# Kernel optimization log

Hardware: AMD Instinct MI355X
Metric: run time of the kernel (lower is better)

## Reference

```python
import jax, jax.numpy as jnp
import numpy as np

N_HEADS = 16
N_KV_HEADS = 4
HEAD_DIM = 128
D_MODEL = 2048
WINDOW = 1024
THETA = 10000.0
EPS = 1e-6


def _rmsnorm(x, w):
    var = jnp.mean(x * x, axis=-1, keepdims=True)
    return x * jax.lax.rsqrt(var + EPS) * w


def _rope(x, pos):
    # x: [B, H, S, D]; rotate-half (llama-style) RoPE
    d2 = HEAD_DIM // 2
    inv_freq = 1.0 / (THETA ** (jnp.arange(0, HEAD_DIM, 2, dtype=jnp.float32) / HEAD_DIM))
    ang = pos[:, None].astype(jnp.float32) * inv_freq[None, :]  # [S, D/2]
    cos = jnp.cos(ang)[None, None]
    sin = jnp.sin(ang)[None, None]
    x1, x2 = x[..., :d2], x[..., d2:]
    return jnp.concatenate([x1 * cos - x2 * sin, x1 * sin + x2 * cos], axis=-1)


def setup_inputs() -> dict:
    key = jax.random.key(0)
    ks = jax.random.split(key, 7)
    B, S = 1, 2048
    s = 0.02
    return {
        "x": jax.random.normal(ks[0], (B, S, D_MODEL), jnp.float32),
        "wq": jax.random.normal(ks[1], (N_HEADS * HEAD_DIM, D_MODEL), jnp.float32) * s,
        "wk": jax.random.normal(ks[2], (N_KV_HEADS * HEAD_DIM, D_MODEL), jnp.float32) * s,
        "wv": jax.random.normal(ks[3], (N_KV_HEADS * HEAD_DIM, D_MODEL), jnp.float32) * s,
        "wo": jax.random.normal(ks[4], (D_MODEL, N_HEADS * HEAD_DIM), jnp.float32) * s,
        "q_norm_w": jnp.ones((HEAD_DIM,), jnp.float32),
        "k_norm_w": jnp.ones((HEAD_DIM,), jnp.float32),
    }


def reference(x, wq, wk, wv, wo, q_norm_w, k_norm_w):
    B, S, _ = x.shape
    past_length = 0
    scale = HEAD_DIM ** -0.5
    n_rep = N_HEADS // N_KV_HEADS

    q = (x @ wq.T).reshape(B, S, N_HEADS, HEAD_DIM).transpose(0, 2, 1, 3)
    k = (x @ wk.T).reshape(B, S, N_KV_HEADS, HEAD_DIM).transpose(0, 2, 1, 3)
    v = (x @ wv.T).reshape(B, S, N_KV_HEADS, HEAD_DIM).transpose(0, 2, 1, 3)

    q = _rmsnorm(q, q_norm_w)
    k = _rmsnorm(k, k_norm_w)

    pos = jnp.arange(S) + past_length
    q = _rope(q, pos)
    k = _rope(k, pos)

    # GQA: materialize repeated KV heads, as in _repeat_kv
    k_rep = jnp.repeat(k, n_rep, axis=1)  # [B, H, S, D]
    v_rep = jnp.repeat(v, n_rep, axis=1)

    # sliding-window causal mask (total_seq_len=S > WINDOW)
    q_idx = jnp.arange(S)[:, None] + past_length
    k_idx = jnp.arange(S)[None, :]
    mask = (q_idx >= k_idx) & (q_idx - k_idx < WINDOW)  # [S, S]

    scores = jnp.einsum("bhqd,bhkd->bhqk", q, k_rep) * scale
    scores = jnp.where(mask[None, None], scores, jnp.float32(-jnp.inf))
    attn = jax.nn.softmax(scores, axis=-1)
    out = jnp.einsum("bhqk,bhkd->bhqd", attn, v_rep)

    out = out.transpose(0, 2, 1, 3).reshape(B, S, N_HEADS * HEAD_DIM)
    return out @ wo.T
```

## Files before the change

kernel.cpp:

```cpp
#include <hip/hip_runtime.h>
#include <hip/hip_bf16.h>
#include <cstdint>
#include <cstddef>

typedef __attribute__((ext_vector_type(4))) float f32x4;
typedef __attribute__((ext_vector_type(8))) short bf16x8;
typedef __attribute__((ext_vector_type(8))) unsigned short us8;

#define MFMA16(a, b, c) __builtin_amdgcn_mfma_f32_16x16x32_bf16(a, b, c, 0, 0, 0)

__device__ inline unsigned short f2bf(float f) {
    unsigned int u = __float_as_uint(f);
    u += 0x7fffu + ((u >> 16) & 1u);
    return (unsigned short)(u >> 16);
}
__device__ inline float bf2f(unsigned short u) {
    return __uint_as_float((unsigned int)u << 16);
}
__device__ inline unsigned short f2bf_fast(float f) {
    float r;
    asm("v_cvt_pk_bf16_f32 %0, %1, %2" : "=v"(r) : "v"(f), "v"(f));
    return (unsigned short)__float_as_uint(r);
}

__device__ inline void gload_lds16(const void* g, void* l) {
    __builtin_amdgcn_global_load_lds(
        (const __attribute__((address_space(1))) void*)g,
        (__attribute__((address_space(3))) void*)l, 16, 0, 0);
}
__device__ inline unsigned lds_addr(const void* p) {
    return (unsigned)(size_t)((__attribute__((address_space(3))) const void*)p);
}

__global__ __launch_bounds__(256) void prep_all(const float* __restrict__ x,
                                                const float* __restrict__ wq,
                                                const float* __restrict__ wk,
                                                const float* __restrict__ wv,
                                                const float* __restrict__ wo,
                                                unsigned short* __restrict__ xb,
                                                unsigned short* __restrict__ wqkv,
                                                unsigned short* __restrict__ wob,
                                                float2* __restrict__ tbl) {
    const int b = blockIdx.x;
    if (b < 14336) {
        const float* src; unsigned short* dst; int off4;
        if (b < 4096)       { src = x;  dst = xb;                 off4 = b; }
        else if (b < 8192)  { src = wq; dst = wqkv;               off4 = b - 4096; }
        else if (b < 9216)  { src = wk; dst = wqkv + 2048 * 2048; off4 = b - 8192; }
        else if (b < 10240) { src = wv; dst = wqkv + 2560 * 2048; off4 = b - 9216; }
        else                { src = wo; dst = wob;                off4 = b - 10240; }
        int i = (off4 * 256 + threadIdx.x) * 4;
        float4 v = *(const float4*)(src + i);
        ushort4 o;
        o.x = f2bf(v.x); o.y = f2bf(v.y); o.z = f2bf(v.z); o.w = f2bf(v.w);
        *(ushort4*)(dst + i) = o;
    } else {
        int idx = (b - 14336) * 256 + threadIdx.x;
        int row = idx >> 6, t = idx & 63;
        float inv_freq = exp2f((float)t * (-2.0f / 128.0f) * 13.287712379549449f);
        float s, c;
        sincosf((float)row * inv_freq, &s, &c);
        tbl[idx] = make_float2(c, s);
    }
}

__global__ __launch_bounds__(512, 1) void gemm256(const unsigned short* __restrict__ A,
                                                  const unsigned short* __restrict__ B,
                                                  unsigned short* __restrict__ Cp,
                                                  int M, int N, int Kfull, int kspan) {
    __shared__ unsigned short As[2][256 * 64];
    __shared__ unsigned short Bs[2][256 * 64];
    const int tid = threadIdx.x;
    const int lane = tid & 63, wave = tid >> 6;
    const int wr = wave >> 2, wc = wave & 3;
    const int l15 = lane & 15, l4 = lane >> 4;
    const int gx = gridDim.x;
    const int nwg = gx * gridDim.y;
    const int bid0 = blockIdx.y * gx + blockIdx.x;
    const int q8 = nwg >> 3, r8 = nwg & 7;
    const int xcd = bid0 & 7, sub = bid0 >> 3;
    const int wgid = ((xcd < r8) ? xcd * (q8 + 1) : r8 * (q8 + 1) + (xcd - r8) * q8) + sub;
    const int bm = wgid / gx, bn = wgid % gx;
    const int z = blockIdx.z;
    const unsigned short* Az = A + (size_t)z * kspan;
    const unsigned short* Bz = B + (size_t)z * kspan;
    unsigned short* C = Cp + (size_t)z * M * N;
    const int nK = kspan >> 6;

    f32x4 acc[8][4] = {};

    const int sA0 = tid, sA1 = 512 + tid, sA2 = 1024 + tid, sA3 = 1536 + tid;
#define SRCOF(s) ((((((s) & 7) * 16) ^ ((((s) >> 3) & 7) << 4)) >> 1))
    const unsigned short* pa0 = Az + (size_t)(bm * 256 + (sA0 >> 3)) * Kfull + SRCOF(sA0);
    const unsigned short* pa1 = Az + (size_t)(bm * 256 + (sA1 >> 3)) * Kfull + SRCOF(sA1);
    const unsigned short* pa2 = Az + (size_t)(bm * 256 + (sA2 >> 3)) * Kfull + SRCOF(sA2);
    const unsigned short* pa3 = Az + (size_t)(bm * 256 + (sA3 >> 3)) * Kfull + SRCOF(sA3);
    const unsigned short* pb0 = Bz + (size_t)(bn * 256 + (sA0 >> 3)) * Kfull + SRCOF(sA0);
    const unsigned short* pb1 = Bz + (size_t)(bn * 256 + (sA1 >> 3)) * Kfull + SRCOF(sA1);
    const unsigned short* pb2 = Bz + (size_t)(bn * 256 + (sA2 >> 3)) * Kfull + SRCOF(sA2);
    const unsigned short* pb3 = Bz + (size_t)(bn * 256 + (sA3 >> 3)) * Kfull + SRCOF(sA3);
#undef SRCOF

#define STG(kt, bb)                                           \
    do {                                                      \
        gload_lds16(pa0 + (kt) * 64, &As[bb][sA0 * 8]);       \
        gload_lds16(pa1 + (kt) * 64, &As[bb][sA1 * 8]);       \
        gload_lds16(pa2 + (kt) * 64, &As[bb][sA2 * 8]);       \
        gload_lds16(pa3 + (kt) * 64, &As[bb][sA3 * 8]);       \
        gload_lds16(pb0 + (kt) * 64, &Bs[bb][sA0 * 8]);       \
        gload_lds16(pb1 + (kt) * 64, &Bs[bb][sA1 * 8]);       \
        gload_lds16(pb2 + (kt) * 64, &Bs[bb][sA2 * 8]);       \
        gload_lds16(pb3 + (kt) * 64, &Bs[bb][sA3 * 8]);       \
    } while (0)

    const unsigned swz = (unsigned)((l4 * 16) ^ ((l15 & 7) << 4));
    const unsigned aB0 = lds_addr(&As[0][0]) + (unsigned)((wr * 128 + l15) * 128) + swz;
    const unsigned aB1 = aB0 ^ 64u;
    const unsigned bB0 = lds_addr(&Bs[0][0]) + (unsigned)((wc * 64 + l15) * 128) + swz;
    const unsigned bB1 = bB0 ^ 64u;

#define DSR(dst, addr, off) \
    asm volatile("ds_read_b128 %0, %1 offset:" #off : "=v"(dst) : "v"(addr))

    STG(0, 0);
    for (int kt = 0; kt < nK; ++kt) {
        const int bc = kt & 1;
        asm volatile("s_waitcnt vmcnt(0)\ns_barrier" ::: "memory");
        __builtin_amdgcn_sched_barrier(0);

        const unsigned aA0 = aB0 + bc * 32768, aA1 = aB1 + bc * 32768;
        const unsigned bA0 = bB0 + bc * 32768, bA1 = bB1 + bc * 32768;
        bf16x8 a00, a01, a02, a03, a04, a05, a06, a07;
        bf16x8 a10, a11, a12, a13, a14, a15, a16, a17;
        bf16x8 b00, b01, b02, b03, b10, b11, b12, b13;

        DSR(b00, bA0, 0);    DSR(b01, bA0, 2048);
        DSR(b02, bA0, 4096); DSR(b03, bA0, 6144);
        DSR(a00, aA0, 0);    DSR(a01, aA0, 2048);
        DSR(a02, aA0, 4096); DSR(a03, aA0, 6144);
        DSR(a04, aA0, 8192);  DSR(a05, aA0, 10240);
        DSR(a06, aA0, 12288); DSR(a07, aA0, 14336);

        if (kt + 1 < nK) STG(kt + 1, bc ^ 1);

        asm volatile("s_waitcnt lgkmcnt(4)" ::: "memory");
        __builtin_amdgcn_sched_barrier(0);
        __builtin_amdgcn_s_setprio(1);
        acc[0][0] = MFMA16(a00, b00, acc[0][0]); acc[0][1] = MFMA16(a00, b01, acc[0][1]);
        acc[0][2] = MFMA16(a00, b02, acc[0][2]); acc[0][3] = MFMA16(a00, b03, acc[0][3]);
        acc[1][0] = MFMA16(a01, b00, acc[1][0]); acc[1][1] = MFMA16(a01, b01, acc[1][1]);
        acc[1][2] = MFMA16(a01, b02, acc[1][2]); acc[1][3] = MFMA16(a01, b03, acc[1][3]);
        acc[2][0] = MFMA16(a02, b00, acc[2][0]); acc[2][1] = MFMA16(a02, b01, acc[2][1]);
        acc[2][2] = MFMA16(a02, b02, acc[2][2]); acc[2][3] = MFMA16(a02, b03, acc[2][3]);
        acc[3][0] = MFMA16(a03, b00, acc[3][0]); acc[3][1] = MFMA16(a03, b01, acc[3][1]);
        acc[3][2] = MFMA16(a03, b02, acc[3][2]); acc[3][3] = MFMA16(a03, b03, acc[3][3]);
        __builtin_amdgcn_s_setprio(0);

        DSR(b10, bA1, 0);    DSR(b11, bA1, 2048);
        DSR(b12, bA1, 4096); DSR(b13, bA1, 6144);
        DSR(a10, aA1, 0);    DSR(a11, aA1, 2048);
        DSR(a12, aA1, 4096); DSR(a13, aA1, 6144);

        asm volatile("s_waitcnt lgkmcnt(8)" ::: "memory");
        __builtin_amdgcn_sched_barrier(0);
        __builtin_amdgcn_s_setprio(1);
        acc[4][0] = MFMA16(a04, b00, acc[4][0]); acc[4][1] = MFMA16(a04, b01, acc[4][1]);
        acc[4][2] = MFMA16(a04, b02, acc[4][2]); acc[4][3] = MFMA16(a04, b03, acc[4][3]);
        acc[5][0] = MFMA16(a05, b00, acc[5][0]); acc[5][1] = MFMA16(a05, b01, acc[5][1]);
        acc[5][2] = MFMA16(a05, b02, acc[5][2]); acc[5][3] = MFMA16(a05, b03, acc[5][3]);
        acc[6][0] = MFMA16(a06, b00, acc[6][0]); acc[6][1] = MFMA16(a06, b01, acc[6][1]);
        acc[6][2] = MFMA16(a06, b02, acc[6][2]); acc[6][3] = MFMA16(a06, b03, acc[6][3]);
        acc[7][0] = MFMA16(a07, b00, acc[7][0]); acc[7][1] = MFMA16(a07, b01, acc[7][1]);
        acc[7][2] = MFMA16(a07, b02, acc[7][2]); acc[7][3] = MFMA16(a07, b03, acc[7][3]);
        __builtin_amdgcn_s_setprio(0);

        DSR(a14, aA1, 8192);  DSR(a15, aA1, 10240);
        DSR(a16, aA1, 12288); DSR(a17, aA1, 14336);

        asm volatile("s_waitcnt lgkmcnt(4)" ::: "memory");
        __builtin_amdgcn_sched_barrier(0);
        __builtin_amdgcn_s_setprio(1);
        acc[0][0] = MFMA16(a10, b10, acc[0][0]); acc[0][1] = MFMA16(a10, b11, acc[0][1]);
        acc[0][2] = MFMA16(a10, b12, acc[0][2]); acc[0][3] = MFMA16(a10, b13, acc[0][3]);
        acc[1][0] = MFMA16(a11, b10, acc[1][0]); acc[1][1] = MFMA16(a11, b11, acc[1][1]);
        acc[1][2] = MFMA16(a11, b12, acc[1][2]); acc[1][3] = MFMA16(a11, b13, acc[1][3]);
        acc[2][0] = MFMA16(a12, b10, acc[2][0]); acc[2][1] = MFMA16(a12, b11, acc[2][1]);
        acc[2][2] = MFMA16(a12, b12, acc[2][2]); acc[2][3] = MFMA16(a12, b13, acc[2][3]);
        acc[3][0] = MFMA16(a13, b10, acc[3][0]); acc[3][1] = MFMA16(a13, b11, acc[3][1]);
        acc[3][2] = MFMA16(a13, b12, acc[3][2]); acc[3][3] = MFMA16(a13, b13, acc[3][3]);
        __builtin_amdgcn_s_setprio(0);

        asm volatile("s_waitcnt lgkmcnt(0)" ::: "memory");
        __builtin_amdgcn_sched_barrier(0);
        __builtin_amdgcn_s_setprio(1);
        acc[4][0] = MFMA16(a14, b10, acc[4][0]); acc[4][1] = MFMA16(a14, b11, acc[4][1]);
        acc[4][2] = MFMA16(a14, b12, acc[4][2]); acc[4][3] = MFMA16(a14, b13, acc[4][3]);
        acc[5][0] = MFMA16(a15, b10, acc[5][0]); acc[5][1] = MFMA16(a15, b11, acc[5][1]);
        acc[5][2] = MFMA16(a15, b12, acc[5][2]); acc[5][3] = MFMA16(a15, b13, acc[5][3]);
        acc[6][0] = MFMA16(a16, b10, acc[6][0]); acc[6][1] = MFMA16(a16, b11, acc[6][1]);
        acc[6][2] = MFMA16(a16, b12, acc[6][2]); acc[6][3] = MFMA16(a16, b13, acc[6][3]);
        acc[7][0] = MFMA16(a17, b10, acc[7][0]); acc[7][1] = MFMA16(a17, b11, acc[7][1]);
        acc[7][2] = MFMA16(a17, b12, acc[7][2]); acc[7][3] = MFMA16(a17, b13, acc[7][3]);
        __builtin_amdgcn_s_setprio(0);
    }
#undef STG
#undef DSR

    for (int m = 0; m < 8; ++m)
        for (int n = 0; n < 4; ++n)
            for (int j = 0; j < 4; ++j) {
                int row = bm * 256 + wr * 128 + m * 16 + l4 * 4 + j;
                int col = bn * 256 + wc * 64 + n * 16 + l15;
                C[(size_t)row * N + col] = f2bf_fast(acc[m][n][j]);
            }
}

__global__ __launch_bounds__(256) void norm_rope(const unsigned short* __restrict__ p0,
                                                 const unsigned short* __restrict__ p1,
                                                 const float* __restrict__ qw,
                                                 const float* __restrict__ kw,
                                                 const float2* __restrict__ tbl,
                                                 unsigned short* __restrict__ Qb,
                                                 unsigned short* __restrict__ Kb) {
    const int row = blockIdx.x;
    const int head = blockIdx.y * 4 + (threadIdx.x >> 6);
    const int t = threadIdx.x & 63;
    const size_t off = (size_t)row * 3072 + head * 128;
    float x1 = bf2f(p0[off + t]) + bf2f(p1[off + t]);
    float x2 = bf2f(p0[off + t + 64]) + bf2f(p1[off + t + 64]);
    float ss = x1 * x1 + x2 * x2;
    for (int m = 32; m; m >>= 1) ss += __shfl_xor(ss, m);
    float r = rsqrtf(ss * (1.0f / 128.0f) + 1e-6f);
    const float* w = (head < 16) ? qw : kw;
    float y1 = x1 * r * w[t], y2 = x2 * r * w[t + 64];
    float2 cs = tbl[row * 64 + t];
    x1 = y1 * cs.x - y2 * cs.y;
    x2 = y1 * cs.y + y2 * cs.x;
    if (head < 16) {
        const float SCALE2 = 0.12751879526654698f;
        x1 *= SCALE2; x2 *= SCALE2;
    }
    unsigned short* dst = (head < 16) ? Qb + ((size_t)head * 2048 + row) * 128
                                      : Kb + ((size_t)(head - 16) * 2048 + row) * 128;
    dst[t] = f2bf(x1);
    dst[t + 64] = f2bf(x2);
}

__global__ __launch_bounds__(256) void transpose_v(const unsigned short* __restrict__ p0,
                                                   const unsigned short* __restrict__ p1,
                                                   unsigned short* __restrict__ VbT) {
    const int kt = blockIdx.x;
    const int h  = blockIdx.y;
    __shared__ unsigned short T[64 * 132];
    const int tid = threadIdx.x;
    for (int i = 0; i < 8; ++i) {
        int s = i * 256 + tid;
        int r = s >> 5, c = (s & 31) * 4;
        size_t off = (size_t)(kt * 64 + r) * 3072 + (20 + h) * 128 + c;
        ushort4 a = *(const ushort4*)(p0 + off);
        ushort4 b = *(const ushort4*)(p1 + off);
        ushort4 o;
        o.x = f2bf(bf2f(a.x) + bf2f(b.x));
        o.y = f2bf(bf2f(a.y) + bf2f(b.y));
        o.z = f2bf(bf2f(a.z) + bf2f(b.z));
        o.w = f2bf(bf2f(a.w) + bf2f(b.w));
        *(ushort4*)&T[r * 132 + c] = o;
    }
    __syncthreads();
    for (int i = 0; i < 4; ++i) {
        int s = i * 256 + tid;
        int d = s >> 3, ck = (s & 7) * 8;
        us8 v;
        for (int j = 0; j < 8; ++j) {
            int c = ck + j;
            int k = (c & 3) * 16 + (c >> 2);
            v[j] = T[k * 132 + d];
        }
        *(us8*)(VbT + (size_t)h * 128 * 2048 + (size_t)d * 2048 + kt * 64 + ck) = v;
    }
}

__global__ __launch_bounds__(512) void attn_fwd(const unsigned short* __restrict__ Qb,
                                                const unsigned short* __restrict__ Kb,
                                                const unsigned short* __restrict__ VbT,
                                                unsigned short* __restrict__ Ob) {
    const int bid = blockIdx.x;
    const int p = bid & 7;
    const int qt = bid >> 3;
    const int q0 = qt * 64;
    __shared__ unsigned short Ks[2][64 * 128];
    __shared__ unsigned short Vs[128 * 64];
    __shared__ char PsB[8][16 * 136];
    const int tid = threadIdx.x;
    const int lane = tid & 63, wave = tid >> 6;
    const int l15 = lane & 15, l4 = lane >> 4;
    const int h = 2 * p + (wave >> 2);
    const int rgrp = wave & 3;
    const int kvh = p >> 1;

    bf16x8 qf[4];
    {
        const unsigned short* qrow =
            Qb + ((size_t)h * 2048 + q0 + rgrp * 16 + l15) * 128 + l4 * 8;
        for (int kk = 0; kk < 4; ++kk) qf[kk] = *(const bf16x8*)(qrow + kk * 32);
    }
    f32x4 o[8] = {};
    float m2[4], lp[4];
    for (int j = 0; j < 4; ++j) { m2[j] = -1e30f; lp[j] = 0.0f; }
    const int kt_lo = (qt >= 16) ? (qt - 16) : 0;

    const unsigned short* Kh = Kb + (size_t)kvh * 2048 * 128;
    const unsigned short* Vh = VbT + (size_t)kvh * 128 * 2048;

    int ksr[2], ksc[2], vsr[2], vsc[2];
    for (int i = 0; i < 2; ++i) {
        int s = i * 512 + tid;
        ksr[i] = s >> 4;
        ksc[i] = (((s & 15) * 16) ^ ((ksr[i] & 7) << 4)) >> 1;
        vsr[i] = s >> 3;
        vsc[i] = (((s & 7) * 16) ^ ((vsr[i] & 7) << 4)) >> 1;
    }

    for (int i = 0; i < 2; ++i)
        gload_lds16(Kh + (size_t)(kt_lo * 64 + ksr[i]) * 128 + ksc[i],
                    &Ks[0][(i * 512 + tid) * 8]);

    int cur = 0;
    for (int kt = kt_lo; kt <= qt; ++kt) {
        asm volatile("s_waitcnt vmcnt(0)\ns_barrier" ::: "memory");
        __builtin_amdgcn_sched_barrier(0);

        for (int i = 0; i < 2; ++i)
            gload_lds16(Vh + (size_t)vsr[i] * 2048 + kt * 64 + vsc[i],
                        &Vs[(i * 512 + tid) * 8]);
        if (kt < qt) {
            for (int i = 0; i < 2; ++i)
                gload_lds16(Kh + (size_t)((kt + 1) * 64 + ksr[i]) * 128 + ksc[i],
                            &Ks[cur ^ 1][(i * 512 + tid) * 8]);
        }

        f32x4 s[4] = {};
        __builtin_amdgcn_s_setprio(1);
        for (int nn = 0; nn < 4; ++nn)
            for (int kk = 0; kk < 4; ++kk) {
                int r = nn * 16 + l15;
                int cb = (kk * 64 + l4 * 16) ^ ((r & 7) << 4);
                bf16x8 kf = *(const bf16x8*)((const char*)&Ks[cur][0] + r * 256 + cb);
                s[nn] = MFMA16(qf[kk], kf, s[nn]);
            }
        __builtin_amdgcn_s_setprio(0);

        float pv4[4][4];
        const bool masked = (kt == qt) || (qt >= 16 && kt == kt_lo);
        if (masked) {
            for (int nn = 0; nn < 4; ++nn) {
                int kc = kt * 64 + nn * 16 + l15;
                for (int j = 0; j < 4; ++j) {
                    int qr = q0 + rgrp * 16 + l4 * 4 + j;
                    unsigned diff = (unsigned)(qr - kc);
                    pv4[nn][j] = (diff < 1024u) ? s[nn][j] : -1e30f;
                }
            }
        } else {
            for (int nn = 0; nn < 4; ++nn)
                for (int j = 0; j < 4; ++j) pv4[nn][j] = s[nn][j];
        }

        float mxl[4];
        bool flag = true;
        for (int j = 0; j < 4; ++j) {
            mxl[j] = fmaxf(fmaxf(pv4[0][j], pv4[1][j]), fmaxf(pv4[2][j], pv4[3][j]));
            flag = flag && (mxl[j] <= m2[j] + 11.0f);
        }
        if (!__all(flag)) {
            for (int j = 0; j < 4; ++j) {
                float mx = mxl[j];
                for (int mk = 8; mk; mk >>= 1) mx = fmaxf(mx, __shfl_xor(mx, mk));
                float mnew = fmaxf(m2[j], mx);
                float corr = exp2f(m2[j] - mnew);
                m2[j] = mnew;
                lp[j] *= corr;
                for (int dd = 0; dd < 8; ++dd) o[dd][j] *= corr;
            }
        }
        for (int j = 0; j < 4; ++j) {
            float rs = 0.0f;
            for (int nn = 0; nn < 4; ++nn) {
                float pv = exp2f(pv4[nn][j] - m2[j]);
                pv4[nn][j] = pv;
                rs += pv;
            }
            lp[j] += rs;
        }

        for (int j = 0; j < 4; ++j) {
            int row = l4 * 4 + j;
            unsigned lo, hi;
            asm("v_cvt_pk_bf16_f32 %0, %1, %2" : "=v"(lo) : "v"(pv4[0][j]), "v"(pv4[1][j]));
            asm("v_cvt_pk_bf16_f32 %0, %1, %2" : "=v"(hi) : "v"(pv4[2][j]), "v"(pv4[3][j]));
            int cb = (l15 * 8) ^ ((row & 7) << 4);
            *(uint2*)(&PsB[wave][0] + row * 136 + cb) = make_uint2(lo, hi);
        }

        bf16x8 pa[2];
        for (int kk2 = 0; kk2 < 2; ++kk2) {
            int cb = (kk2 * 64 + l4 * 16) ^ ((l15 & 7) << 4);
            pa[kk2] = *(const bf16x8*)(&PsB[wave][0] + l15 * 136 + cb);
        }

        if (kt < qt)
            asm volatile("s_waitcnt vmcnt(2)\ns_barrier" ::: "memory");
        else
            asm volatile("s_waitcnt vmcnt(0)\ns_barrier" ::: "memory");
        __builtin_amdgcn_sched_barrier(0);

        __builtin_amdgcn_s_setprio(1);
        for (int dd = 0; dd < 8; ++dd)
            for (int kk2 = 0; kk2 < 2; ++kk2) {
                int d = dd * 16 + l15;
                int cb = (kk2 * 64 + l4 * 16) ^ ((d & 7) << 4);
                bf16x8 vf = *(const bf16x8*)((const char*)&Vs[0] + d * 128 + cb);
                o[dd] = MFMA16(pa[kk2], vf, o[dd]);
            }
        __builtin_amdgcn_s_setprio(0);
        cur ^= 1;
    }

    for (int j = 0; j < 4; ++j) {
        float lt = lp[j];
        for (int mk = 8; mk; mk >>= 1) lt += __shfl_xor(lt, mk);
        float inv = 1.0f / lt;
        int row = q0 + rgrp * 16 + l4 * 4 + j;
        unsigned short* orow = Ob + (size_t)row * 2048 + h * 128;
        for (int dd = 0; dd < 8; ++dd) orow[dd * 16 + l15] = f2bf_fast(o[dd][j] * inv);
    }
}

__global__ __launch_bounds__(256) void add4(const unsigned short* __restrict__ p,
                                            float* __restrict__ out, int n) {
    int i = (blockIdx.x * 256 + threadIdx.x) * 8;
    if (i >= n) return;
    us8 a = *(const us8*)(p + i);
    us8 b = *(const us8*)(p + 4194304 + i);
    us8 c = *(const us8*)(p + 8388608 + i);
    us8 d = *(const us8*)(p + 12582912 + i);
    f32x4 o0, o1;
    for (int j = 0; j < 4; ++j)
        o0[j] = (bf2f(a[j]) + bf2f(b[j])) + (bf2f(c[j]) + bf2f(d[j]));
    for (int j = 0; j < 4; ++j)
        o1[j] = (bf2f(a[j + 4]) + bf2f(b[j + 4])) + (bf2f(c[j + 4]) + bf2f(d[j + 4]));
    *(f32x4*)(out + i) = o0;
    *(f32x4*)(out + i + 4) = o1;
}

extern "C" void kernel_launch(void* const* d_in, const int* in_sizes, int n_in,
                              void* d_out, int out_size, void* d_ws, size_t ws_size,
                              hipStream_t stream) {
    const float* x  = (const float*)d_in[0];
    const float* wq = (const float*)d_in[1];
    const float* wk = (const float*)d_in[2];
    const float* wv = (const float*)d_in[3];
    const float* wo = (const float*)d_in[4];
    const float* qw = (const float*)d_in[5];
    const float* kw = (const float*)d_in[6];
    float* out = (float*)d_out;

    char* ws = (char*)d_ws;
    unsigned short* xb   = (unsigned short*)(ws + 0);
    unsigned short* wqkv = (unsigned short*)(ws + 8388608);
    unsigned short* wob  = (unsigned short*)(ws + 20971520);
    unsigned short* qkvP = (unsigned short*)(ws + 29360128);
    unsigned short* Qb   = (unsigned short*)(ws + 54525952);
    unsigned short* Kb   = (unsigned short*)(ws + 62914560);
    unsigned short* VbT  = (unsigned short*)(ws + 65011712);
    unsigned short* Ob   = (unsigned short*)(ws + 67108864);
    unsigned short* outP = (unsigned short*)(ws + 29360128);
    float2*         tbl  = (float2*)(ws + 104857600);

    prep_all<<<dim3(14848), dim3(256), 0, stream>>>(x, wq, wk, wv, wo, xb, wqkv, wob, tbl);
    gemm256<<<dim3(12, 8, 2), dim3(512), 0, stream>>>(xb, wqkv, qkvP, 2048, 3072, 2048, 1024);
    norm_rope<<<dim3(2048, 5), dim3(256), 0, stream>>>(qkvP, qkvP + 2048 * 3072, qw, kw, tbl, Qb, Kb);
    transpose_v<<<dim3(32, 4), dim3(256), 0, stream>>>(qkvP, qkvP + 2048 * 3072, VbT);
    attn_fwd<<<dim3(256), dim3(512), 0, stream>>>(Qb, Kb, VbT, Ob);
    gemm256<<<dim3(8, 8, 4), dim3(512), 0, stream>>>(Ob, wob, outP, 2048, 2048, 2048, 512);
    add4<<<dim3(2048), dim3(256), 0, stream>>>(outP, out, 2048 * 2048);
}
```

Baseline: 123.6 us.

## Fuse QK RMSNorm and RoPE into a 128-row QKV GEMM epilogue, dropping split-K

Replaces the split-K QKV GEMM, which wrote two bf16 partial buffers, with a full-K GEMM using 128x256 tiles on a 12x16 grid. Its epilogue applies RMSNorm, RoPE and the Q scale in place and writes Q, K and V straight into head-major buffers, so the separate norm_rope kernel and the partial-sum reads disappear. transpose_v now reads one contiguous head-major V buffer with 16-byte loads. In exchange the GEMM loses the split-K parallelism, each tile runs the full K loop, and the epilogue adds LDS round trips and an intermediate bf16 rounding before RoPE.

```diff
diff --git a/kernel.cpp b/kernel.cpp
--- a/kernel.cpp
+++ b/kernel.cpp
@@ -64,12 +64,177 @@
     }
 }
 
+__global__ __launch_bounds__(512, 1) void gemm_qkv128(const unsigned short* __restrict__ A,
+                                                      const unsigned short* __restrict__ B,
+                                                      const float* __restrict__ qw,
+                                                      const float* __restrict__ kw,
+                                                      const float2* __restrict__ tbl,
+                                                      unsigned short* __restrict__ Qb,
+                                                      unsigned short* __restrict__ Kb,
+                                                      unsigned short* __restrict__ Vb) {
+    constexpr int K = 2048;
+    constexpr int nK = K >> 6;
+    __shared__ __align__(16) char sm[98304];
+    unsigned short* AsB = (unsigned short*)sm;
+    unsigned short* BsB = AsB + 16384;
+    const int tid = threadIdx.x;
+    const int lane = tid & 63, wave = tid >> 6;
+    const int wr = wave >> 2, wc = wave & 3;
+    const int l15 = lane & 15, l4 = lane >> 4;
+    const int gx = gridDim.x;
+    const int nwg = gx * gridDim.y;
+    const int bid0 = blockIdx.y * gx + blockIdx.x;
+    const int q8 = nwg >> 3, r8 = nwg & 7;
+    const int xcd = bid0 & 7, sub = bid0 >> 3;
+    const int wgid = ((xcd < r8) ? xcd * (q8 + 1) : r8 * (q8 + 1) + (xcd - r8) * q8) + sub;
+    const int bm = wgid / gx, bn = wgid % gx;
+
+    f32x4 acc[4][4] = {};
+
+    const int sa0 = tid, sa1 = 512 + tid;
+    const int sb2 = 1024 + tid, sb3 = 1536 + tid;
+#define SRCOF(s) ((((((s) & 7) * 16) ^ ((((s) >> 3) & 7) << 4)) >> 1))
+    const unsigned short* pa0 = A + (size_t)(bm * 128 + (sa0 >> 3)) * K + SRCOF(sa0);
+    const unsigned short* pa1 = A + (size_t)(bm * 128 + (sa1 >> 3)) * K + SRCOF(sa1);
+    const unsigned short* pb0 = B + (size_t)(bn * 256 + (sa0 >> 3)) * K + SRCOF(sa0);
+    const unsigned short* pb1 = B + (size_t)(bn * 256 + (sa1 >> 3)) * K + SRCOF(sa1);
+    const unsigned short* pb2 = B + (size_t)(bn * 256 + (sb2 >> 3)) * K + SRCOF(sb2);
+    const unsigned short* pb3 = B + (size_t)(bn * 256 + (sb3 >> 3)) * K + SRCOF(sb3);
+#undef SRCOF
+
+#define STG(kt, bb)                                              \
+    do {                                                         \
+        gload_lds16(pa0 + (kt) * 64, AsB + (bb) * 8192 + sa0 * 8);  \
+        gload_lds16(pa1 + (kt) * 64, AsB + (bb) * 8192 + sa1 * 8);  \
+        gload_lds16(pb0 + (kt) * 64, BsB + (bb) * 16384 + sa0 * 8); \
+        gload_lds16(pb1 + (kt) * 64, BsB + (bb) * 16384 + sa1 * 8); \
+        gload_lds16(pb2 + (kt) * 64, BsB + (bb) * 16384 + sb2 * 8); \
+        gload_lds16(pb3 + (kt) * 64, BsB + (bb) * 16384 + sb3 * 8); \
+    } while (0)
+
+    const unsigned swz = (unsigned)((l4 * 16) ^ ((l15 & 7) << 4));
+    const unsigned aB0 = lds_addr(AsB) + (unsigned)((wr * 64 + l15) * 128) + swz;
+    const unsigned bB0 = lds_addr(BsB) + (unsigned)((wc * 64 + l15) * 128) + swz;
+
+#define DSR(dst, addr, off) \
+    asm volatile("ds_read_b128 %0, %1 offset:" #off : "=v"(dst) : "v"(addr))
+
+    STG(0, 0);
+    for (int kt = 0; kt < nK; ++kt) {
+        const int bc = kt & 1;
+        asm volatile("s_waitcnt vmcnt(0)\ns_barrier" ::: "memory");
+        __builtin_amdgcn_sched_barrier(0);
+
+        const unsigned aA0 = aB0 + bc * 16384, aA1 = aA0 ^ 64u;
+        const unsigned bA0 = bB0 + bc * 32768, bA1 = bA0 ^ 64u;
+        bf16x8 a00, a01, a02, a03, a10, a11, a12, a13;
+        bf16x8 b00, b01, b02, b03, b10, b11, b12, b13;
+
+        DSR(b00, bA0, 0);    DSR(b01, bA0, 2048);
+        DSR(b02, bA0, 4096); DSR(b03, bA0, 6144);
+        DSR(a00, aA0, 0);    DSR(a01, aA0, 2048);
+        DSR(a02, aA0, 4096); DSR(a03, aA0, 6144);
+        DSR(b10, bA1, 0);    DSR(b11, bA1, 2048);
+        DSR(b12, bA1, 4096); DSR(b13, bA1, 6144);
+        DSR(a10, aA1, 0);    DSR(a11, aA1, 2048);
+        DSR(a12, aA1, 4096); DSR(a13, aA1, 6144);
+
+        if (kt + 1 < nK) STG(kt + 1, bc ^ 1);
+
+        asm volatile("s_waitcnt lgkmcnt(8)" ::: "memory");
+        __builtin_amdgcn_sched_barrier(0);
+        __builtin_amdgcn_s_setprio(1);
+        acc[0][0] = MFMA16(a00, b00, acc[0][0]); acc[0][1] = MFMA16(a00, b01, acc[0][1]);
+        acc[0][2] = MFMA16(a00, b02, acc[0][2]); acc[0][3] = MFMA16(a00, b03, acc[0][3]);
+        acc[1][0] = MFMA16(a01, b00, acc[1][0]); acc[1][1] = MFMA16(a01, b01, acc[1][1]);
+        acc[1][2] = MFMA16(a01, b02, acc[1][2]); acc[1][3] = MFMA16(a01, b03, acc[1][3]);
+        acc[2][0] = MFMA16(a02, b00, acc[2][0]); acc[2][1] = MFMA16(a02, b01, acc[2][1]);
+        acc[2][2] = MFMA16(a02, b02, acc[2][2]); acc[2][3] = MFMA16(a02, b03, acc[2][3]);
+        acc[3][0] = MFMA16(a03, b00, acc[3][0]); acc[3][1] = MFMA16(a03, b01, acc[3][1]);
+        acc[3][2] = MFMA16(a03, b02, acc[3][2]); acc[3][3] = MFMA16(a03, b03, acc[3][3]);
+        __builtin_amdgcn_s_setprio(0);
+
+        asm volatile("s_waitcnt lgkmcnt(0)" ::: "memory");
+        __builtin_amdgcn_sched_barrier(0);
+        __builtin_amdgcn_s_setprio(1);
+        acc[0][0] = MFMA16(a10, b10, acc[0][0]); acc[0][1] = MFMA16(a10, b11, acc[0][1]);
+        acc[0][2] = MFMA16(a10, b12, acc[0][2]); acc[0][3] = MFMA16(a10, b13, acc[0][3]);
+        acc[1][0] = MFMA16(a11, b10, acc[1][0]); acc[1][1] = MFMA16(a11, b11, acc[1][1]);
+        acc[1][2] = MFMA16(a11, b12, acc[1][2]); acc[1][3] = MFMA16(a11, b13, acc[1][3]);
+        acc[2][0] = MFMA16(a12, b10, acc[2][0]); acc[2][1] = MFMA16(a12, b11, acc[2][1]);
+        acc[2][2] = MFMA16(a12, b12, acc[2][2]); acc[2][3] = MFMA16(a12, b13, acc[2][3]);
+        acc[3][0] = MFMA16(a13, b10, acc[3][0]); acc[3][1] = MFMA16(a13, b11, acc[3][1]);
+        acc[3][2] = MFMA16(a13, b12, acc[3][2]); acc[3][3] = MFMA16(a13, b13, acc[3][3]);
+        __builtin_amdgcn_s_setprio(0);
+    }
+#undef STG
+#undef DSR
+
+    const int hl = wc >> 1;
+    const int half = wc & 1;
+    __syncthreads();
+
+    if (bn >= 10) {
+        const int head_v = 2 * bn - 20 + hl;
+        unsigned short* dst = Vb + (size_t)head_v * 2048 * 128;
+        for (int m = 0; m < 4; ++m)
+            for (int j = 0; j < 4; ++j) {
+                int row = bm * 128 + wr * 64 + m * 16 + l4 * 4 + j;
+                for (int n = 0; n < 4; ++n)
+                    dst[(size_t)row * 128 + half * 64 + n * 16 + l15] = f2bf_fast(acc[m][n][j]);
+            }
+        return;
+    }
+
+    unsigned short* ybuf = (unsigned short*)sm;
+    float* ssbuf = (float*)(sm + 67584);
+    for (int m = 0; m < 4; ++m)
+        for (int j = 0; j < 4; ++j) {
+            float ss = 0.0f;
+            for (int n = 0; n < 4; ++n) ss += acc[m][n][j] * acc[m][n][j];
+            for (int mk = 8; mk; mk >>= 1) ss += __shfl_xor(ss, mk);
+            if (l15 == 0) ssbuf[wc * 128 + wr * 64 + m * 16 + l4 * 4 + j] = ss;
+        }
+    __syncthreads();
+    const float* w = (bn < 8) ? qw : kw;
+    float wv4[4];
+    for (int n = 0; n < 4; ++n) wv4[n] = w[half * 64 + n * 16 + l15];
+    for (int m = 0; m < 4; ++m)
+        for (int j = 0; j < 4; ++j) {
+            int lrow = wr * 64 + m * 16 + l4 * 4 + j;
+            float tot = ssbuf[hl * 256 + lrow] + ssbuf[hl * 256 + 128 + lrow];
+            float rr = rsqrtf(tot * (1.0f / 128.0f) + 1e-6f);
+            for (int n = 0; n < 4; ++n)
+                ybuf[lrow * 264 + wc * 64 + n * 16 + l15] = f2bf(acc[m][n][j] * rr * wv4[n]);
+        }
+    __syncthreads();
+    const int head_g = 2 * bn + hl;
+    unsigned short* dstbase = (bn < 8) ? Qb + (size_t)head_g * 2048 * 128
+                                       : Kb + (size_t)(head_g - 16) * 2048 * 128;
+    const float SCALE2 = 0.12751879526654698f;
+    for (int m = 0; m < 4; ++m)
+        for (int j = 0; j < 4; ++j) {
+            int lrow = wr * 64 + m * 16 + l4 * 4 + j;
+            int grow = bm * 128 + lrow;
+            for (int n = 0; n < 4; ++n) {
+                int wcol = wc * 64 + n * 16 + l15;
+                float2 cs = tbl[grow * 64 + (wcol & 63)];
+                float own = bf2f(ybuf[lrow * 264 + wcol]);
+                float par = bf2f(ybuf[lrow * 264 + (wcol ^ 64)]);
+                float outv = (half == 0) ? own * cs.x - par * cs.y
+                                         : par * cs.y + own * cs.x;
+                if (bn < 8) outv *= SCALE2;
+                dstbase[(size_t)grow * 128 + (wcol & 127)] = f2bf(outv);
+            }
+        }
+}
+
 __global__ __launch_bounds__(512, 1) void gemm256(const unsigned short* __restrict__ A,
                                                   const unsigned short* __restrict__ B,
                                                   unsigned short* __restrict__ Cp,
                                                   int M, int N, int Kfull, int kspan) {
-    __shared__ unsigned short As[2][256 * 64];
-    __shared__ unsigned short Bs[2][256 * 64];
+    __shared__ unsigned short As[2][16384];
+    __shared__ unsigned short Bs[2][16384];
     const int tid = threadIdx.x;
     const int lane = tid & 63, wave = tid >> 6;
     const int wr = wave >> 2, wc = wave & 3;
@@ -101,23 +266,21 @@
     const unsigned short* pb3 = Bz + (size_t)(bn * 256 + (sA3 >> 3)) * Kfull + SRCOF(sA3);
 #undef SRCOF
 
-#define STG(kt, bb)                                           \
-    do {                                                      \
-        gload_lds16(pa0 + (kt) * 64, &As[bb][sA0 * 8]);       \
-        gload_lds16(pa1 + (kt) * 64, &As[bb][sA1 * 8]);       \
-        gload_lds16(pa2 + (kt) * 64, &As[bb][sA2 * 8]);       \
-        gload_lds16(pa3 + (kt) * 64, &As[bb][sA3 * 8]);       \
-        gload_lds16(pb0 + (kt) * 64, &Bs[bb][sA0 * 8]);       \
-        gload_lds16(pb1 + (kt) * 64, &Bs[bb][sA1 * 8]);       \
-        gload_lds16(pb2 + (kt) * 64, &Bs[bb][sA2 * 8]);       \
-        gload_lds16(pb3 + (kt) * 64, &Bs[bb][sA3 * 8]);       \
+#define STG(kt, bb)                                            \
+    do {                                                       \
+        gload_lds16(pa0 + (kt) * 64, &As[bb][sA0 * 8]);        \
+        gload_lds16(pa1 + (kt) * 64, &As[bb][sA1 * 8]);        \
+        gload_lds16(pa2 + (kt) * 64, &As[bb][sA2 * 8]);        \
+        gload_lds16(pa3 + (kt) * 64, &As[bb][sA3 * 8]);        \
+        gload_lds16(pb0 + (kt) * 64, &Bs[bb][sA0 * 8]);        \
+        gload_lds16(pb1 + (kt) * 64, &Bs[bb][sA1 * 8]);        \
+        gload_lds16(pb2 + (kt) * 64, &Bs[bb][sA2 * 8]);        \
+        gload_lds16(pb3 + (kt) * 64, &Bs[bb][sA3 * 8]);        \
     } while (0)
 
     const unsigned swz = (unsigned)((l4 * 16) ^ ((l15 & 7) << 4));
     const unsigned aB0 = lds_addr(&As[0][0]) + (unsigned)((wr * 128 + l15) * 128) + swz;
-    const unsigned aB1 = aB0 ^ 64u;
     const unsigned bB0 = lds_addr(&Bs[0][0]) + (unsigned)((wc * 64 + l15) * 128) + swz;
-    const unsigned bB1 = bB0 ^ 64u;
 
 #define DSR(dst, addr, off) \
     asm volatile("ds_read_b128 %0, %1 offset:" #off : "=v"(dst) : "v"(addr))
@@ -128,8 +291,10 @@
         asm volatile("s_waitcnt vmcnt(0)\ns_barrier" ::: "memory");
         __builtin_amdgcn_sched_barrier(0);
 
-        const unsigned aA0 = aB0 + bc * 32768, aA1 = aB1 + bc * 32768;
-        const unsigned bA0 = bB0 + bc * 32768, bA1 = bB1 + bc * 32768;
+        const unsigned aA0 = aB0 + bc * 32768;
+        const unsigned aA1 = aA0 ^ 64u;
+        const unsigned bA0 = bB0 + bc * 32768;
+        const unsigned bA1 = bA0 ^ 64u;
         bf16x8 a00, a01, a02, a03, a04, a05, a06, a07;
         bf16x8 a10, a11, a12, a13, a14, a15, a16, a17;
         bf16x8 b00, b01, b02, b03, b10, b11, b12, b13;
@@ -215,56 +380,17 @@
             }
 }
 
-__global__ __launch_bounds__(256) void norm_rope(const unsigned short* __restrict__ p0,
-                                                 const unsigned short* __restrict__ p1,
-                                                 const float* __restrict__ qw,
-                                                 const float* __restrict__ kw,
-                                                 const float2* __restrict__ tbl,
-                                                 unsigned short* __restrict__ Qb,
-                                                 unsigned short* __restrict__ Kb) {
-    const int row = blockIdx.x;
-    const int head = blockIdx.y * 4 + (threadIdx.x >> 6);
-    const int t = threadIdx.x & 63;
-    const size_t off = (size_t)row * 3072 + head * 128;
-    float x1 = bf2f(p0[off + t]) + bf2f(p1[off + t]);
-    float x2 = bf2f(p0[off + t + 64]) + bf2f(p1[off + t + 64]);
-    float ss = x1 * x1 + x2 * x2;
-    for (int m = 32; m; m >>= 1) ss += __shfl_xor(ss, m);
-    float r = rsqrtf(ss * (1.0f / 128.0f) + 1e-6f);
-    const float* w = (head < 16) ? qw : kw;
-    float y1 = x1 * r * w[t], y2 = x2 * r * w[t + 64];
-    float2 cs = tbl[row * 64 + t];
-    x1 = y1 * cs.x - y2 * cs.y;
-    x2 = y1 * cs.y + y2 * cs.x;
-    if (head < 16) {
-        const float SCALE2 = 0.12751879526654698f;
-        x1 *= SCALE2; x2 *= SCALE2;
-    }
-    unsigned short* dst = (head < 16) ? Qb + ((size_t)head * 2048 + row) * 128
-                                      : Kb + ((size_t)(head - 16) * 2048 + row) * 128;
-    dst[t] = f2bf(x1);
-    dst[t + 64] = f2bf(x2);
-}
-
-__global__ __launch_bounds__(256) void transpose_v(const unsigned short* __restrict__ p0,
-                                                   const unsigned short* __restrict__ p1,
+__global__ __launch_bounds__(256) void transpose_v(const unsigned short* __restrict__ Vb,
                                                    unsigned short* __restrict__ VbT) {
     const int kt = blockIdx.x;
     const int h  = blockIdx.y;
     __shared__ unsigned short T[64 * 132];
     const int tid = threadIdx.x;
-    for (int i = 0; i < 8; ++i) {
+    for (int i = 0; i < 4; ++i) {
         int s = i * 256 + tid;
-        int r = s >> 5, c = (s & 31) * 4;
-        size_t off = (size_t)(kt * 64 + r) * 3072 + (20 + h) * 128 + c;
-        ushort4 a = *(const ushort4*)(p0 + off);
-        ushort4 b = *(const ushort4*)(p1 + off);
-        ushort4 o;
-        o.x = f2bf(bf2f(a.x) + bf2f(b.x));
-        o.y = f2bf(bf2f(a.y) + bf2f(b.y));
-        o.z = f2bf(bf2f(a.z) + bf2f(b.z));
-        o.w = f2bf(bf2f(a.w) + bf2f(b.w));
-        *(ushort4*)&T[r * 132 + c] = o;
+        int r = s >> 4, c = (s & 15) * 8;
+        us8 v = *(const us8*)(Vb + ((size_t)h * 2048 + kt * 64 + r) * 128 + c);
+        *(us8*)&T[r * 132 + c] = v;
     }
     __syncthreads();
     for (int i = 0; i < 4; ++i) {
@@ -469,18 +595,17 @@
     unsigned short* xb   = (unsigned short*)(ws + 0);
     unsigned short* wqkv = (unsigned short*)(ws + 8388608);
     unsigned short* wob  = (unsigned short*)(ws + 20971520);
-    unsigned short* qkvP = (unsigned short*)(ws + 29360128);
+    unsigned short* Vb   = (unsigned short*)(ws + 29360128);
     unsigned short* Qb   = (unsigned short*)(ws + 54525952);
     unsigned short* Kb   = (unsigned short*)(ws + 62914560);
     unsigned short* VbT  = (unsigned short*)(ws + 65011712);
     unsigned short* Ob   = (unsigned short*)(ws + 67108864);
-    unsigned short* outP = (unsigned short*)(ws + 29360128);
+    unsigned short* outP = (unsigned short*)(ws + 31457280);
     float2*         tbl  = (float2*)(ws + 104857600);
 
     prep_all<<<dim3(14848), dim3(256), 0, stream>>>(x, wq, wk, wv, wo, xb, wqkv, wob, tbl);
-    gemm256<<<dim3(12, 8, 2), dim3(512), 0, stream>>>(xb, wqkv, qkvP, 2048, 3072, 2048, 1024);
-    norm_rope<<<dim3(2048, 5), dim3(256), 0, stream>>>(qkvP, qkvP + 2048 * 3072, qw, kw, tbl, Qb, Kb);
-    transpose_v<<<dim3(32, 4), dim3(256), 0, stream>>>(qkvP, qkvP + 2048 * 3072, VbT);
+    gemm_qkv128<<<dim3(12, 16), dim3(512), 0, stream>>>(xb, wqkv, qw, kw, tbl, Qb, Kb, Vb);
+    transpose_v<<<dim3(32, 4), dim3(256), 0, stream>>>(Vb, VbT);
     attn_fwd<<<dim3(256), dim3(512), 0, stream>>>(Qb, Kb, VbT, Ob);
     gemm256<<<dim3(8, 8, 4), dim3(512), 0, stream>>>(Ob, wob, outP, 2048, 2048, 2048, 512);
     add4<<<dim3(2048), dim3(256), 0, stream>>>(outP, out, 2048 * 2048);
```

Measured after the change: 126.9 us. 1.03x slower.
